# Kernel tuning notes

Hardware: AMD Instinct MI355X
Metric: run time of the kernel (lower is better)

## Reference

```python
import jax, jax.numpy as jnp
import numpy as np

B, T, V, H, O = 256, 1024, 128, 128, 2  # batch, max_len, input_size, hidden, n_outputs


def setup_inputs() -> dict:
    key = jax.random.key(0)
    ks = jax.random.split(key, 9)
    # ragged one-hot sequences: symbol 0 is the pad symbol
    lengths = jax.random.randint(ks[0], (B,), 1, T + 1)
    symbols = jax.random.randint(ks[1], (B, T), 1, V)  # real symbols in [1, V)
    t_idx = jnp.arange(T)[None, :]
    symbols = jnp.where(t_idx < lengths[:, None], symbols, 0)  # pad tail with symbol 0
    x = jax.nn.one_hot(symbols, V, dtype=jnp.float32)  # [B, T, V]
    # RNN params (torch nn.RNN layout: W_ih [H, V-1], W_hh [H, H])
    s = 1.0 / np.sqrt(H)
    W_ih = jax.random.uniform(ks[2], (H, V - 1), minval=-s, maxval=s)
    W_hh = jax.random.uniform(ks[3], (H, H), minval=-s, maxval=s)
    b_ih = jax.random.uniform(ks[4], (H,), minval=-s, maxval=s)
    b_hh = jax.random.uniform(ks[5], (H,), minval=-s, maxval=s)
    # dense head: Linear(H, O)
    W_out = jax.random.uniform(ks[6], (O, H), minval=-s, maxval=s)
    b_out = jax.random.uniform(ks[7], (O,), minval=-s, maxval=s)
    return {"x": x, "W_ih": W_ih, "W_hh": W_hh, "b_ih": b_ih,
            "b_hh": b_hh, "W_out": W_out, "b_out": b_out}


def reference(x, W_ih, W_hh, b_ih, b_hh, W_out, b_out):
    Bk, Tk, Vk = x.shape
    # unpad: length = first timestep whose argmax is the pad symbol (index 0)
    is_pad = jnp.argmax(x, axis=-1) == 0  # [B, T]
    length = jnp.where(is_pad.any(-1), jnp.argmax(is_pad, axis=-1), Tk)  # [B]
    active = jnp.arange(Tk)[None, :] < length[:, None]  # [B, T]
    feats = x[..., 1:]  # strip pad column -> [B, T, V-1]
    # precompute input projection for all timesteps (streaming part)
    pre = jnp.einsum('btf,hf->bth', feats, W_ih) + b_ih + b_hh  # [B, T, H]

    def step(h, inp):
        pre_t, act_t = inp  # [B, H], [B]
        h_new = jnp.tanh(pre_t + h @ W_hh.T)
        h = jnp.where(act_t[:, None], h_new, h)  # freeze hidden past each seq's length
        return h, None

    h0 = jnp.zeros((Bk, W_hh.shape[0]), dtype=x.dtype)
    h_last, _ = jax.lax.scan(step, h0, (pre.transpose(1, 0, 2), active.T))
    fed = jax.nn.softmax(h_last @ W_out.T + b_out, axis=-1)  # [B, O]
    hidden = h_last[None]  # [1, B, H], matches torch stacked layer hidden
    return fed, hidden
```

## Files before the change

kernel.cpp:

```cpp
#include <hip/hip_runtime.h>
#include <stdint.h>

#define Bsz   256
#define Tlen  1024
#define Vocab 128
#define Hdim  128
#define NTHR  256
#define WTN   ((Vocab - 1) * Hdim)

#define CHD   20
#define HBUFI (4 * CHD)

typedef _Float16 half2_t __attribute__((ext_vector_type(2)));

__device__ __forceinline__ float tanh_fast(float x) {
    float e = __builtin_amdgcn_exp2f(x * 2.885390081777927f);
    return 1.0f - 2.0f * __builtin_amdgcn_rcpf(e + 1.0f);
}

__device__ __forceinline__ float dpp_xor1(float s) {
    return __int_as_float(__builtin_amdgcn_mov_dpp(__float_as_int(s), 0xB1, 0xF, 0xF, true));
}
__device__ __forceinline__ float dpp_xor2(float s) {
    return __int_as_float(__builtin_amdgcn_mov_dpp(__float_as_int(s), 0x4E, 0xF, 0xF, true));
}

__global__ __launch_bounds__(256) void transpose_kernel(
    const float* __restrict__ W_ih, float* __restrict__ wt)
{
    int idx = blockIdx.x * 256 + threadIdx.x;
    if (idx < WTN) {
        int h = idx / (Vocab - 1);
        int f = idx - h * (Vocab - 1);
        wt[f * Hdim + h] = W_ih[idx];
    }
}

__global__ __launch_bounds__(NTHR, 1) void rnn_kernel(
    const float* __restrict__ x, const float* __restrict__ wt,
    const float* __restrict__ W_hh,
    const float* __restrict__ b_ih, const float* __restrict__ b_hh,
    const float* __restrict__ W_out, const float* __restrict__ b_out,
    float* __restrict__ out)
{
    __shared__ float wt_s[WTN];
    __shared__ int   syms[Tlen];
    __shared__ __align__(16) int hbuf[2][HBUFI];
    __shared__ int   len_sh;

    const int tid = threadIdx.x;
    const int b   = blockIdx.x;
    const int g   = tid >> 2;
    const int j   = tid & 3;

    if (tid == 0) len_sh = Tlen;
    if (tid < 2 * HBUFI) ((int*)hbuf)[tid] = 0;

    int wp[32];
    #pragma unroll
    for (int r = 0; r < 2; r++) {
        const float4* wrow = (const float4*)(W_hh + (2 * g + r) * Hdim + 32 * j);
        #pragma unroll
        for (int q4 = 0; q4 < 8; q4++) {
            float4 t4 = wrow[q4];
            wp[r * 16 + q4 * 2 + 0] = __builtin_bit_cast(int, __builtin_amdgcn_cvt_pkrtz(t4.x, t4.y));
            wp[r * 16 + q4 * 2 + 1] = __builtin_bit_cast(int, __builtin_amdgcn_cvt_pkrtz(t4.z, t4.w));
        }
    }
    const float bias0 = b_ih[2 * g]     + b_hh[2 * g];
    const float bias1 = b_ih[2 * g + 1] + b_hh[2 * g + 1];

    {
        const float4* src = (const float4*)wt;
        float4* dst = (float4*)wt_s;
        for (int k = tid; k < WTN / 4; k += NTHR) dst[k] = src[k];
    }

    {
        const float4* xb = (const float4*)(x + (size_t)b * Tlen * Vocab);
        const int R4 = Tlen * Vocab / 4;
        for (int base = 0; base < R4; base += NTHR * 8) {
            float4 v[8];
            #pragma unroll
            for (int i = 0; i < 8; i++) v[i] = xb[base + NTHR * i + tid];
            #pragma unroll
            for (int i = 0; i < 8; i++) {
                int k = base + NTHR * i + tid;
                int c = -1;
                if      (v[i].x > 0.5f) c = 0;
                else if (v[i].y > 0.5f) c = 1;
                else if (v[i].z > 0.5f) c = 2;
                else if (v[i].w > 0.5f) c = 3;
                if (c >= 0) syms[k >> 5] = ((k & 31) << 2) + c;
            }
        }
    }
    __syncthreads();

    {
        int lm = Tlen;
        for (int k = tid; k < Tlen; k += NTHR)
            if (syms[k] == 0 && k < lm) lm = k;
        if (lm < Tlen) atomicMin(&len_sh, lm);
    }
    __syncthreads();
    const int len = len_sh;

    const float2* wt2 = (const float2*)wt_s;
    float2 pre_v = {0.0f, 0.0f}, p_t1 = {0.0f, 0.0f};
    int s_t2 = 1;
    if (len > 0) pre_v = wt2[(syms[0] - 1) * 64 + g];
    if (len > 1) p_t1  = wt2[(syms[1] - 1) * 64 + g];
    if (len > 2) s_t2  = syms[2];

    const char* hb0 = (const char*)hbuf[0];
    const char* hb1 = (const char*)hbuf[1];
    const int roff = j * (CHD * 4);
    const int widx = CHD * (g >> 4) + (g & 15);

    for (int t = 0; t < len; t++) {
        #pragma unroll
        for (int k = 0; k < 32; k += 8)
            asm volatile("" : "+v"(wp[k]), "+v"(wp[k+1]), "+v"(wp[k+2]), "+v"(wp[k+3]),
                              "+v"(wp[k+4]), "+v"(wp[k+5]), "+v"(wp[k+6]), "+v"(wp[k+7]));

        const char* hb = (t & 1) ? hb1 : hb0;
        uint4 r0 = *(const uint4*)(hb + roff);
        uint4 r1 = *(const uint4*)(hb + roff + 16);
        uint4 r2 = *(const uint4*)(hb + roff + 32);
        uint4 r3 = *(const uint4*)(hb + roff + 48);

        float2 p_t2 = wt2[(s_t2 - 1) * 64 + g];
        int   s_t3 = (t + 3 < len) ? syms[t + 3] : 1;

        unsigned hr[16] = {r0.x, r0.y, r0.z, r0.w, r1.x, r1.y, r1.z, r1.w,
                           r2.x, r2.y, r2.z, r2.w, r3.x, r3.y, r3.z, r3.w};

        float a00 = 0.0f, a01 = 0.0f, a10 = 0.0f, a11 = 0.0f;
        #pragma unroll
        for (int d = 0; d < 8; d++) {
            half2_t h0 = __builtin_bit_cast(half2_t, hr[d]);
            half2_t h1 = __builtin_bit_cast(half2_t, hr[8 + d]);
            a00 = __builtin_amdgcn_fdot2(h0, __builtin_bit_cast(half2_t, wp[d]),      a00, false);
            a01 = __builtin_amdgcn_fdot2(h1, __builtin_bit_cast(half2_t, wp[8 + d]),  a01, false);
            a10 = __builtin_amdgcn_fdot2(h0, __builtin_bit_cast(half2_t, wp[16 + d]), a10, false);
            a11 = __builtin_amdgcn_fdot2(h1, __builtin_bit_cast(half2_t, wp[24 + d]), a11, false);
        }
        float a0 = a00 + a01, a1 = a10 + a11;
        a0 += dpp_xor1(a0); a1 += dpp_xor1(a1);
        a0 += dpp_xor2(a0); a1 += dpp_xor2(a1);

        float h0 = tanh_fast(a0 + pre_v.x + bias0);
        float h1 = tanh_fast(a1 + pre_v.y + bias1);
        int pk = __builtin_bit_cast(int, __builtin_amdgcn_cvt_pkrtz(h0, h1));
        if (j == 0) ((int*)hbuf[(t + 1) & 1])[widx] = pk;

        pre_v = p_t1; p_t1 = p_t2; s_t2 = s_t3;
        __syncthreads();
    }

    const _Float16* hf = (const _Float16*)hbuf[len & 1];
    #define HGET(e) ((float)hf[40 * ((e) >> 5) + (((e) >> 1) & 15) * 2 + ((e) & 1)])
    if (tid < Hdim)
        out[2 * Bsz + b * Hdim + tid] = HGET(tid);
    if (tid < 64) {
        float h0 = HGET(tid);
        float h1 = HGET(tid + 64);
        float p0 = W_out[tid] * h0 + W_out[64 + tid] * h1;
        float p1 = W_out[128 + tid] * h0 + W_out[192 + tid] * h1;
        #pragma unroll
        for (int off = 32; off > 0; off >>= 1) {
            p0 += __shfl_down(p0, off, 64);
            p1 += __shfl_down(p1, off, 64);
        }
        if (tid == 0) {
            float l0 = p0 + b_out[0], l1 = p1 + b_out[1];
            float m  = fmaxf(l0, l1);
            float e0 = __expf(l0 - m), e1 = __expf(l1 - m);
            float d  = e0 + e1;
            out[b * 2 + 0] = e0 / d;
            out[b * 2 + 1] = e1 / d;
        }
    }
    #undef HGET
}

extern "C" void kernel_launch(void* const* d_in, const int* in_sizes, int n_in,
                              void* d_out, int out_size, void* d_ws, size_t ws_size,
                              hipStream_t stream) {
    const float* x     = (const float*)d_in[0];
    const float* W_ih  = (const float*)d_in[1];
    const float* W_hh  = (const float*)d_in[2];
    const float* b_ih  = (const float*)d_in[3];
    const float* b_hh  = (const float*)d_in[4];
    const float* W_out = (const float*)d_in[5];
    const float* b_out = (const float*)d_in[6];
    float* out = (float*)d_out;

    float* wt = (float*)d_ws;

    const int NTRN = (WTN + 255) / 256;
    transpose_kernel<<<NTRN, 256, 0, stream>>>(W_ih, wt);
    rnn_kernel<<<Bsz, NTHR, 0, stream>>>(x, wt, W_hh, b_ih, b_hh, W_out, b_out, out);
}
```

Baseline: 453.5 us.

## Fuse W_ih transpose into RNN kernel and read x only up to length

Drops the separate transpose kernel: each block now transposes W_ih into padded shared memory and folds the bias sum into it. Sequence length is found first by scanning column 0 of x, so the one-hot read is limited to the active rows instead of the whole 1024-step sequence. This cuts a kernel launch, removes the bias add from the recurrent loop, and skips reading padded x rows. In exchange every block repeats the transpose with strided shared-memory stores.

```diff
diff --git a/kernel.cpp b/kernel.cpp
--- a/kernel.cpp
+++ b/kernel.cpp
@@ -7,6 +7,7 @@
 #define Hdim  128
 #define NTHR  256
 #define WTN   ((Vocab - 1) * Hdim)
+#define WTS   130
 
 #define CHD   20
 #define HBUFI (4 * CHD)
@@ -25,25 +26,15 @@
     return __int_as_float(__builtin_amdgcn_mov_dpp(__float_as_int(s), 0x4E, 0xF, 0xF, true));
 }
 
-__global__ __launch_bounds__(256) void transpose_kernel(
-    const float* __restrict__ W_ih, float* __restrict__ wt)
-{
-    int idx = blockIdx.x * 256 + threadIdx.x;
-    if (idx < WTN) {
-        int h = idx / (Vocab - 1);
-        int f = idx - h * (Vocab - 1);
-        wt[f * Hdim + h] = W_ih[idx];
-    }
-}
-
 __global__ __launch_bounds__(NTHR, 1) void rnn_kernel(
-    const float* __restrict__ x, const float* __restrict__ wt,
+    const float* __restrict__ x, const float* __restrict__ W_ih,
     const float* __restrict__ W_hh,
     const float* __restrict__ b_ih, const float* __restrict__ b_hh,
     const float* __restrict__ W_out, const float* __restrict__ b_out,
     float* __restrict__ out)
 {
-    __shared__ float wt_s[WTN];
+    __shared__ float wt_s[(Vocab - 1) * WTS];
+    __shared__ float bsum_s[Hdim];
     __shared__ int   syms[Tlen];
     __shared__ __align__(16) int hbuf[2][HBUFI];
     __shared__ int   len_sh;
@@ -55,6 +46,20 @@
 
     if (tid == 0) len_sh = Tlen;
     if (tid < 2 * HBUFI) ((int*)hbuf)[tid] = 0;
+    if (tid < Hdim) bsum_s[tid] = b_ih[tid] + b_hh[tid];
+
+    {
+        const float* xcol = x + (size_t)b * Tlen * Vocab;
+        int lm = Tlen;
+        for (int t = tid; t < Tlen; t += NTHR)
+            if (xcol[(size_t)t * Vocab] > 0.5f && t < lm) lm = t;
+        #pragma unroll
+        for (int off = 32; off > 0; off >>= 1) {
+            int o = __shfl_xor(lm, off, 64);
+            if (o < lm) lm = o;
+        }
+        if ((tid & 63) == 0 && lm < Tlen) atomicMin(&len_sh, lm);
+    }
 
     int wp[32];
     #pragma unroll
@@ -67,22 +72,36 @@
             wp[r * 16 + q4 * 2 + 1] = __builtin_bit_cast(int, __builtin_amdgcn_cvt_pkrtz(t4.z, t4.w));
         }
     }
-    const float bias0 = b_ih[2 * g]     + b_hh[2 * g];
-    const float bias1 = b_ih[2 * g + 1] + b_hh[2 * g + 1];
+
+    __syncthreads();
+    const int len = len_sh;
 
     {
-        const float4* src = (const float4*)wt;
-        float4* dst = (float4*)wt_s;
-        for (int k = tid; k < WTN / 4; k += NTHR) dst[k] = src[k];
+        const float4* w4 = (const float4*)W_ih;
+        for (int k4 = tid; k4 < WTN / 4; k4 += NTHR) {
+            float4 v = w4[k4];
+            int k = 4 * k4;
+            #pragma unroll
+            for (int e = 0; e < 4; e++) {
+                int ke = k + e;
+                int h  = ke / (Vocab - 1);
+                int f  = ke - h * (Vocab - 1);
+                float val = (e == 0) ? v.x : (e == 1) ? v.y : (e == 2) ? v.z : v.w;
+                wt_s[f * WTS + h] = val + bsum_s[h];
+            }
+        }
     }
 
     {
         const float4* xb = (const float4*)(x + (size_t)b * Tlen * Vocab);
-        const int R4 = Tlen * Vocab / 4;
-        for (int base = 0; base < R4; base += NTHR * 8) {
+        const int rows4 = len << 5;
+        for (int base = 0; base < rows4; base += NTHR * 8) {
             float4 v[8];
             #pragma unroll
-            for (int i = 0; i < 8; i++) v[i] = xb[base + NTHR * i + tid];
+            for (int i = 0; i < 8; i++) {
+                int k = base + NTHR * i + tid;
+                v[i] = (k < rows4) ? xb[k] : make_float4(0.f, 0.f, 0.f, 0.f);
+            }
             #pragma unroll
             for (int i = 0; i < 8; i++) {
                 int k = base + NTHR * i + tid;
@@ -97,20 +116,11 @@
     }
     __syncthreads();
 
-    {
-        int lm = Tlen;
-        for (int k = tid; k < Tlen; k += NTHR)
-            if (syms[k] == 0 && k < lm) lm = k;
-        if (lm < Tlen) atomicMin(&len_sh, lm);
-    }
-    __syncthreads();
-    const int len = len_sh;
-
     const float2* wt2 = (const float2*)wt_s;
     float2 pre_v = {0.0f, 0.0f}, p_t1 = {0.0f, 0.0f};
     int s_t2 = 1;
-    if (len > 0) pre_v = wt2[(syms[0] - 1) * 64 + g];
-    if (len > 1) p_t1  = wt2[(syms[1] - 1) * 64 + g];
+    if (len > 0) pre_v = wt2[(syms[0] - 1) * (WTS / 2) + g];
+    if (len > 1) p_t1  = wt2[(syms[1] - 1) * (WTS / 2) + g];
     if (len > 2) s_t2  = syms[2];
 
     const char* hb0 = (const char*)hbuf[0];
@@ -130,7 +140,7 @@
         uint4 r2 = *(const uint4*)(hb + roff + 32);
         uint4 r3 = *(const uint4*)(hb + roff + 48);
 
-        float2 p_t2 = wt2[(s_t2 - 1) * 64 + g];
+        float2 p_t2 = wt2[(s_t2 - 1) * (WTS / 2) + g];
         int   s_t3 = (t + 3 < len) ? syms[t + 3] : 1;
 
         unsigned hr[16] = {r0.x, r0.y, r0.z, r0.w, r1.x, r1.y, r1.z, r1.w,
@@ -150,9 +160,9 @@
         a0 += dpp_xor1(a0); a1 += dpp_xor1(a1);
         a0 += dpp_xor2(a0); a1 += dpp_xor2(a1);
 
-        float h0 = tanh_fast(a0 + pre_v.x + bias0);
-        float h1 = tanh_fast(a1 + pre_v.y + bias1);
-        int pk = __builtin_bit_cast(int, __builtin_amdgcn_cvt_pkrtz(h0, h1));
+        float h0v = tanh_fast(a0 + pre_v.x);
+        float h1v = tanh_fast(a1 + pre_v.y);
+        int pk = __builtin_bit_cast(int, __builtin_amdgcn_cvt_pkrtz(h0v, h1v));
         if (j == 0) ((int*)hbuf[(t + 1) & 1])[widx] = pk;
 
         pre_v = p_t1; p_t1 = p_t2; s_t2 = s_t3;
@@ -197,9 +207,5 @@
     const float* b_out = (const float*)d_in[6];
     float* out = (float*)d_out;
 
-    float* wt = (float*)d_ws;
-
-    const int NTRN = (WTN + 255) / 256;
-    transpose_kernel<<<NTRN, 256, 0, stream>>>(W_ih, wt);
-    rnn_kernel<<<Bsz, NTHR, 0, stream>>>(x, wt, W_hh, b_ih, b_hh, W_out, b_out, out);
-}
+    rnn_kernel<<<Bsz, NTHR, 0, stream>>>(x, W_ih, W_hh, b_ih, b_hh, W_out, b_out, out);
+}
```

Measured after the change: 487.1 us. 7.4% more time.
